# Kernel optimization log

Hardware: AMD Instinct MI355X
Metric: run time of the kernel (lower is better)

## Reference

```python
import jax, jax.numpy as jnp
import numpy as np

H, W = 256, 256
S, S_IDX, END_BIAS = 48, 3, 10
E_IDX = S - END_BIAS          # 38
N_ITER = E_IDX - (S_IDX + 1)  # 34 sequential segments after the start segment
OUT_WIN = 10                  # outlier1d window length
OUT_THRESH = 2.0


def setup_inputs() -> dict:
    key = jax.random.key(0)
    # (x, y) event coordinates in [0, W) x [0, H); t/p/b columns are unused by the module.
    events = jax.random.uniform(key, (16, 960000, 2), jnp.float32, minval=0.0, maxval=256.0)
    return {"events": events}


def _blur(a):
    """5x5 uniform (0.04) blur, SAME padding; a: [B, S, D] -> [B, S, D]."""
    k = jnp.full((1, 1, 5, 5), 0.04, jnp.float32)
    return jax.lax.conv_general_dilated(a[:, None], k, (1, 1), [(2, 2), (2, 2)])[:, 0]


def _outlier_flags(m):
    """outlier1d(m[b, si:si+10], thresh=2)[0] for si in [S_IDX+1, E_IDX). m: [B,S] -> bool [B,N_ITER]."""
    widx = (jnp.arange(N_ITER)[:, None] + S_IDX + 1) + jnp.arange(OUT_WIN)[None, :]
    w = m[:, widx]                                   # [B, N_ITER, 10]
    med = jnp.median(w, axis=-1, keepdims=True)
    diff = jnp.abs(w - med)
    mad = jnp.median(diff, axis=-1)                  # [B, N_ITER]
    return 0.6745 * diff[..., 0] / mad > OUT_THRESH


def reference(events):
    B, N, _ = events.shape
    segmentLen = N // S            # static python int
    Nu = segmentLen * S
    x = events[:, :Nu, 0].astype(jnp.int32)   # [B, Nu]
    y = events[:, :Nu, 1].astype(jnp.int32)
    chunks = jnp.repeat(jnp.arange(S), segmentLen)   # segment id per event, [Nu]
    bidx = jnp.arange(B)[:, None]

    # per-batch x-t / y-t histograms via scatter-add
    alongX = jnp.zeros((B, S, W), jnp.float32).at[bidx, chunks[None, :], x].add(1.0)
    alongY = jnp.zeros((B, S, H), jnp.float32).at[bidx, chunks[None, :], y].add(1.0)

    def proc_axis(along, D):
        flat = along.reshape(B, -1)
        cv = (flat.mean(-1) + 3.0 * jnp.std(flat, axis=-1, ddof=1))[:, None, None]
        a = _blur(jnp.clip(along, 0.0, cv))
        m = jnp.einsum('bsd,d->bs', a, jnp.arange(D, dtype=jnp.float32)) / segmentLen
        start = m[:, S_IDX:S_IDX + 1]
        aligned = jnp.round(m - start - (D // 2 - start)).astype(jnp.int32)
        return m, aligned

    meanX, alignedX = proc_axis(alongX, W)
    meanY, alignedY = proc_axis(alongY, H)
    is_out = _outlier_flags(meanX) | _outlier_flags(meanY)   # [B, N_ITER]

    def per_batch(xb, yb, aX, aY, outb):
        xs = jnp.clip(xb - aX[chunks], 0, W - 1)
        ys = jnp.clip(yb - aY[chunks], 0, H - 1)
        idx_c = (xs + W * ys).reshape(S, segmentLen)
        idx_v = (xs // 2 + (W // 2) * (ys // 2)).reshape(S, segmentLen)
        container0 = jnp.zeros(W * H, jnp.int32).at[idx_c[S_IDX]].add(1)
        ver0 = jnp.zeros((W // 2) * (H // 2), bool).at[idx_v[S_IDX]].set(True)

        def step(carry, inp):
            container, ver, stopped = carry
            ic, iv, is_o = inp
            ver_new = ver.at[iv].set(True)
            cnt = jnp.sum(ver_new).astype(jnp.float32)
            new_info = jnp.sum(jnp.logical_xor(ver_new, ver)).astype(jnp.float32)
            brk = new_info / cnt < 0.1
            do = (~stopped) & (~is_o) & (~brk)
            stopped = stopped | ((~stopped) & (~is_o) & brk)
            container = jnp.where(do, container.at[ic].add(1), container)
            ver = jnp.where(do, ver_new, ver)
            return (container, ver, stopped), None

        (container, _, _), _ = jax.lax.scan(
            step, (container0, ver0, jnp.array(False)),
            (idx_c[S_IDX + 1:E_IDX], idx_v[S_IDX + 1:E_IDX], outb))
        c = container.astype(jnp.float32)
        cv = c.mean() + 3.0 * jnp.std(c, ddof=1)
        return jnp.clip(c, 0.0, cv) / cv

    containers = jax.vmap(per_batch)(x, y, alignedX, alignedY, is_out)  # [B, W*H]
    return containers.reshape(B, 1, H, W)
```

## Files before the change

kernel.cpp:

```cpp
#include <hip/hip_runtime.h>

#define NB 16
#define NEV 960000
#define NS 48
#define SEG 20000
#define S_IDX 3
#define E_IDX 38
#define N_ITER 34
#define ND 256
#define NCH 35

__global__ __launch_bounds__(256) void hist_kernel(const float* __restrict__ events,
                                                   float* __restrict__ alongX,
                                                   float* __restrict__ alongY,
                                                   unsigned* __restrict__ compact,
                                                   unsigned* __restrict__ container,
                                                   unsigned long long* __restrict__ sums) {
    __shared__ unsigned hx[4][ND], hy[4][ND];
    int tid = threadIdx.x;
    int blk = blockIdx.x;
    int b = blk / NS, c = blk % NS;
    int wave = tid >> 6;
    #pragma unroll
    for (int j = 0; j < 4; j++) { hx[j][tid] = 0; hy[j][tid] = 0; }
    {
        uint4 z = {0u, 0u, 0u, 0u};
        for (int i = blk * 256 + tid; i < 262144; i += NB * NS * 256)
            ((uint4*)container)[i] = z;
        if (blk == 0 && tid < NB * 2) sums[tid] = 0ull;
    }
    __syncthreads();
    size_t base = (size_t)b * NEV + (size_t)c * SEG;
    const float4* ev4 = (const float4*)(events + base * 2);
    bool wr = (c >= S_IDX && c < E_IDX);
    uint2* dst = wr ? (uint2*)(compact + ((size_t)b * NCH + (c - S_IDX)) * (SEG / 2)) : nullptr;
    unsigned* HX = hx[wave];
    unsigned* HY = hy[wave];
    for (int k = tid; k < SEG / 4; k += 256) {
        float4 v0 = ev4[2 * k], v1 = ev4[2 * k + 1];
        int x0 = (int)v0.x, y0 = (int)v0.y, x1 = (int)v0.z, y1 = (int)v0.w;
        int x2 = (int)v1.x, y2 = (int)v1.y, x3 = (int)v1.z, y3 = (int)v1.w;
        x0 = x0 > 255 ? 255 : x0; y0 = y0 > 255 ? 255 : y0;
        x1 = x1 > 255 ? 255 : x1; y1 = y1 > 255 ? 255 : y1;
        x2 = x2 > 255 ? 255 : x2; y2 = y2 > 255 ? 255 : y2;
        x3 = x3 > 255 ? 255 : x3; y3 = y3 > 255 ? 255 : y3;
        atomicAdd(&HX[x0], 1u); atomicAdd(&HY[y0], 1u);
        atomicAdd(&HX[x1], 1u); atomicAdd(&HY[y1], 1u);
        atomicAdd(&HX[x2], 1u); atomicAdd(&HY[y2], 1u);
        atomicAdd(&HX[x3], 1u); atomicAdd(&HY[y3], 1u);
        if (wr) {
            uint2 p;
            p.x = (unsigned)(x0 | (y0 << 8)) | ((unsigned)(x1 | (y1 << 8)) << 16);
            p.y = (unsigned)(x2 | (y2 << 8)) | ((unsigned)(x3 | (y3 << 8)) << 16);
            dst[k] = p;
        }
    }
    __syncthreads();
    unsigned sx = hx[0][tid] + hx[1][tid] + hx[2][tid] + hx[3][tid];
    unsigned sy = hy[0][tid] + hy[1][tid] + hy[2][tid] + hy[3][tid];
    int o = (b * NS + c) * ND + tid;
    alongX[o] = (float)sx;
    alongY[o] = (float)sy;
}

__global__ __launch_bounds__(256) void stats_kernel(const float* __restrict__ alongX,
                                                    const float* __restrict__ alongY,
                                                    int* __restrict__ alignedX,
                                                    int* __restrict__ alignedY,
                                                    float* __restrict__ m_all) {
    __shared__ float sbuf[NS * ND];
    __shared__ double sredA[4], sredB[4];
    __shared__ float scv;
    int tid = threadIdx.x;
    int b = blockIdx.x >> 1, axis = blockIdx.x & 1;
    const float* along = (axis ? alongY : alongX) + (size_t)b * NS * ND;
    for (int k = 0; k < NS; k++) sbuf[k * ND + tid] = along[k * ND + tid];
    __syncthreads();
    double s = 0.0, s2 = 0.0;
    for (int k = 0; k < NS; k++) { double v = sbuf[k * ND + tid]; s += v; s2 += v * v; }
    for (int off = 32; off; off >>= 1) { s += __shfl_down(s, off); s2 += __shfl_down(s2, off); }
    if ((tid & 63) == 0) { sredA[tid >> 6] = s; sredB[tid >> 6] = s2; }
    __syncthreads();
    if (tid == 0) {
        double ts = sredA[0] + sredA[1] + sredA[2] + sredA[3];
        double ts2 = sredB[0] + sredB[1] + sredB[2] + sredB[3];
        const double N = (double)(NS * ND);
        double mean = ts / N;
        double var  = (ts2 - ts * ts / N) / (N - 1.0);
        scv = (float)(mean + 3.0 * sqrt(var));
    }
    __syncthreads();
    float cv = scv;
    int wave = tid >> 6, lane = tid & 63;
    for (int q = 0; q < 12; ++q) {
        int sI = wave * 12 + q;
        double acc = 0.0;
        #pragma unroll
        for (int k = 0; k < 4; ++k) {
            int d = lane + 64 * k;
            int lo = d - 2 < 0 ? 0 : d - 2;
            int hi = d + 2 > 255 ? 255 : d + 2;
            double Wd = 0.5 * (double)(lo + hi) * (double)(hi - lo + 1);
            double t = 0.0;
            #pragma unroll
            for (int ds = -2; ds <= 2; ++ds) {
                int ss = sI + ds;
                if (ss >= 0 && ss < NS) t += (double)fminf(sbuf[ss * ND + d], cv);
            }
            acc += t * Wd;
        }
        for (int off = 32; off; off >>= 1) acc += __shfl_down(acc, off);
        if (lane == 0) {
            float mf = (float)(acc * 0.04 / (double)SEG);
            m_all[(b * 2 + axis) * NS + sI] = mf;
            (axis ? alignedY : alignedX)[b * NS + sI] = (int)rintf(mf - 128.0f);
        }
    }
}

__global__ __launch_bounds__(256) void mask_kernel(const unsigned* __restrict__ compact,
                                                   const int* __restrict__ alignedX,
                                                   const int* __restrict__ alignedY,
                                                   unsigned* __restrict__ masks) {
    __shared__ unsigned sm[512];
    int tid = threadIdx.x, blk = blockIdx.x;
    int b = blk / NCH, ci = blk % NCH, si = S_IDX + ci;
    sm[tid] = 0; sm[tid + 256] = 0;
    __syncthreads();
    int aX = alignedX[b * NS + si], aY = alignedY[b * NS + si];
    const uint4* cp = (const uint4*)(compact + ((size_t)b * NCH + ci) * (SEG / 2));
    for (int i = tid; i < SEG / 8; i += 256) {
        uint4 w = cp[i];
        unsigned ws[4] = {w.x, w.y, w.z, w.w};
        #pragma unroll
        for (int j = 0; j < 4; j++) {
            unsigned v = ws[j];
            #pragma unroll
            for (int h = 0; h < 2; h++) {
                unsigned e = (h ? (v >> 16) : v) & 0xFFFFu;
                int xs = (int)(e & 255u) - aX; xs = xs < 0 ? 0 : (xs > 255 ? 255 : xs);
                int ys = (int)(e >> 8)   - aY; ys = ys < 0 ? 0 : (ys > 255 ? 255 : ys);
                int iv = (xs >> 1) | ((ys >> 1) << 7);
                atomicOr(&sm[iv >> 5], 1u << (iv & 31));
            }
        }
    }
    __syncthreads();
    unsigned* mo = masks + (size_t)blk * 512;
    mo[tid] = sm[tid];
    mo[tid + 256] = sm[tid + 256];
}

__device__ inline float median10(const float* v) {
    float w[10];
    #pragma unroll
    for (int i = 0; i < 10; i++) w[i] = v[i];
    #pragma unroll
    for (int i = 1; i < 10; i++) {
        float k = w[i]; int j = i - 1;
        while (j >= 0 && w[j] > k) { w[j + 1] = w[j]; j--; }
        w[j + 1] = k;
    }
    return 0.5f * (w[4] + w[5]);
}

__device__ inline bool outlier_flag(const float* w) {
    float med = median10(w);
    float d[10];
    #pragma unroll
    for (int i = 0; i < 10; i++) d[i] = fabsf(w[i] - med);
    float d0 = d[0];
    float mad = median10(d);
    return (0.6745f * d0 / mad) > 2.0f;
}

__device__ inline unsigned wave_sum_u32(unsigned v) {
    for (int off = 32; off; off >>= 1) v += __shfl_xor(v, off);
    return v;
}

__global__ __launch_bounds__(64) void decide_kernel(const unsigned* __restrict__ masks,
                                                    const float* __restrict__ m_all,
                                                    unsigned long long* __restrict__ commitmask) {
    int b = blockIdx.x, lane = threadIdx.x;
    const unsigned* mb = masks + (size_t)b * NCH * 512;
    uint4 v0 = ((const uint4*)mb)[lane * 2];
    uint4 v1 = ((const uint4*)mb)[lane * 2 + 1];
    const uint4* pp = (const uint4*)(mb + 512);
    uint4 p0 = pp[lane * 2], p1 = pp[lane * 2 + 1];
    bool f = false;
    if (lane < N_ITER) {
        const float* mx = m_all + b * 2 * NS;
        const float* my = mx + NS;
        f = outlier_flag(&mx[S_IDX + 1 + lane]) || outlier_flag(&my[S_IDX + 1 + lane]);
    }
    unsigned long long omask = __ballot(f);
    unsigned ver[8] = {v0.x, v0.y, v0.z, v0.w, v1.x, v1.y, v1.z, v1.w};
    unsigned pc = 0;
    #pragma unroll
    for (int j = 0; j < 8; j++) pc += __popc(ver[j]);
    unsigned cnt = wave_sum_u32(pc);
    unsigned long long cm = 1ull;
    for (int idx = 1; idx < NCH; ++idx) {
        uint4 c0 = p0, c1 = p1;
        if (idx + 1 < NCH) {
            const uint4* np = (const uint4*)(mb + (size_t)(idx + 1) * 512);
            p0 = np[lane * 2]; p1 = np[lane * 2 + 1];
        }
        unsigned del[8] = {c0.x, c0.y, c0.z, c0.w, c1.x, c1.y, c1.z, c1.w};
        unsigned nl = 0;
        #pragma unroll
        for (int j = 0; j < 8; j++) nl += __popc(del[j] & ~ver[j]);
        unsigned ni = wave_sum_u32(nl);
        bool is_o = (omask >> (idx - 1)) & 1;
        if (!is_o) {
            unsigned cn = cnt + ni;
            float ratio = (float)ni / (float)cn;
            if (ratio < 0.1f) break;
            cm |= 1ull << idx;
            cnt = cn;
            #pragma unroll
            for (int j = 0; j < 8; j++) ver[j] |= del[j];
        }
    }
    if (lane == 0) commitmask[b] = cm;
}

__global__ __launch_bounds__(256) void commit_kernel(const unsigned* __restrict__ compact,
                                                     const int* __restrict__ alignedX,
                                                     const int* __restrict__ alignedY,
                                                     const unsigned long long* __restrict__ commitmask,
                                                     unsigned* __restrict__ container) {
    int blk = blockIdx.x, tid = threadIdx.x;
    int b = blk / NCH, ci = blk % NCH;
    if (!((commitmask[b] >> ci) & 1ull)) return;
    int si = S_IDX + ci;
    int aX = alignedX[b * NS + si], aY = alignedY[b * NS + si];
    unsigned* cont = container + (size_t)b * 65536;
    const uint4* cp = (const uint4*)(compact + ((size_t)b * NCH + ci) * (SEG / 2));
    for (int i = tid; i < SEG / 8; i += 256) {
        uint4 w = cp[i];
        unsigned ws[4] = {w.x, w.y, w.z, w.w};
        #pragma unroll
        for (int j = 0; j < 4; j++) {
            unsigned v = ws[j];
            #pragma unroll
            for (int h = 0; h < 2; h++) {
                unsigned e = (h ? (v >> 16) : v) & 0xFFFFu;
                int xs = (int)(e & 255u) - aX; xs = xs < 0 ? 0 : (xs > 255 ? 255 : xs);
                int ys = (int)(e >> 8)   - aY; ys = ys < 0 ? 0 : (ys > 255 ? 255 : ys);
                atomicAdd(&cont[xs | (ys << 8)], 1u);
            }
        }
    }
}

__global__ __launch_bounds__(256) void cv_kernel(const unsigned* __restrict__ container,
                                                 unsigned long long* __restrict__ sums) {
    __shared__ unsigned long long sredA[4], sredB[4];
    int tid = threadIdx.x, blk = blockIdx.x;
    int b = blk >> 4, part = blk & 15;
    const uint4* c4 = (const uint4*)(container + (size_t)b * 65536) + part * 1024;
    unsigned long long s = 0, s2 = 0;
    for (int i = tid; i < 1024; i += 256) {
        uint4 v = c4[i];
        s  += (unsigned long long)v.x + v.y + v.z + v.w;
        s2 += (unsigned long long)v.x * v.x + (unsigned long long)v.y * v.y
            + (unsigned long long)v.z * v.z + (unsigned long long)v.w * v.w;
    }
    for (int off = 32; off; off >>= 1) { s += __shfl_down(s, off); s2 += __shfl_down(s2, off); }
    if ((tid & 63) == 0) { sredA[tid >> 6] = s; sredB[tid >> 6] = s2; }
    __syncthreads();
    if (tid == 0) {
        atomicAdd(&sums[b * 2],     sredA[0] + sredA[1] + sredA[2] + sredA[3]);
        atomicAdd(&sums[b * 2 + 1], sredB[0] + sredB[1] + sredB[2] + sredB[3]);
    }
}

__global__ __launch_bounds__(256) void finish_kernel(const unsigned* __restrict__ container,
                                                     const unsigned long long* __restrict__ sums,
                                                     float* __restrict__ out) {
    int g = blockIdx.x * 256 + threadIdx.x;
    int b = g >> 14;
    double ts  = (double)sums[b * 2];
    double ts2 = (double)sums[b * 2 + 1];
    double mean = ts / 65536.0;
    double var  = (ts2 - ts * ts / 65536.0) / 65535.0;
    float cv = (float)(mean + 3.0 * sqrt(var));
    uint4 v = ((const uint4*)container)[g];
    float4 o;
    o.x = fminf((float)v.x, cv) / cv;
    o.y = fminf((float)v.y, cv) / cv;
    o.z = fminf((float)v.z, cv) / cv;
    o.w = fminf((float)v.w, cv) / cv;
    ((float4*)out)[g] = o;
}

extern "C" void kernel_launch(void* const* d_in, const int* in_sizes, int n_in,
                              void* d_out, int out_size, void* d_ws, size_t ws_size,
                              hipStream_t stream) {
    const float* events = (const float*)d_in[0];
    float* out = (float*)d_out;
    char* ws = (char*)d_ws;

    float*    alongX    = (float*)(ws);
    float*    alongY    = (float*)(ws + 786432);
    unsigned* container = (unsigned*)(ws + 1572864);
    int*      alignedX  = (int*)(ws + 5767168);
    int*      alignedY  = (int*)(ws + 5770240);
    float*    m_all     = (float*)(ws + 5773312);
    unsigned long long* commitmask = (unsigned long long*)(ws + 5779456);
    unsigned long long* sums       = (unsigned long long*)(ws + 5779584);
    unsigned* compact   = (unsigned*)(ws + 6291456);
    unsigned* masks     = (unsigned*)(ws + 29360128);

    hist_kernel<<<NB * NS, 256, 0, stream>>>(events, alongX, alongY, compact, container, sums);
    stats_kernel<<<NB * 2, 256, 0, stream>>>(alongX, alongY, alignedX, alignedY, m_all);
    mask_kernel<<<NB * NCH, 256, 0, stream>>>(compact, alignedX, alignedY, masks);
    decide_kernel<<<NB, 64, 0, stream>>>(masks, m_all, commitmask);
    commit_kernel<<<NB * NCH, 256, 0, stream>>>(compact, alignedX, alignedY, commitmask, container);
    cv_kernel<<<NB * 16, 256, 0, stream>>>(container, sums);
    finish_kernel<<<1024, 256, 0, stream>>>(container, sums, out);
}
```

Baseline: 281.1 us.

## Fuse all pipeline stages into one cooperative kernel with grid syncs

Replaces the seven separate kernel launches (histogram, stats, mask, decide, commit, cv, finish) with a single cooperative kernel of 512 persistent blocks. The stages are separated by grid-wide synchronisation, and blocks loop over tiles inside each stage. The goal is to remove per-launch overhead and the gaps between dependent kernels. In exchange, it adds grid-sync cost, leaves many blocks idle during small stages such as stats and decide, and gives the histogram stage an uneven split of 768 tiles over 512 blocks. The old multi-kernel path is kept as a fallback when the occupancy check fails.

```diff
diff --git a/kernel.cpp b/kernel.cpp
--- a/kernel.cpp
+++ b/kernel.cpp
@@ -1,4 +1,7 @@
 #include <hip/hip_runtime.h>
+#include <hip/hip_cooperative_groups.h>
+
+namespace cg = cooperative_groups;
 
 #define NB 16
 #define NEV 960000
@@ -9,6 +12,294 @@
 #define N_ITER 34
 #define ND 256
 #define NCH 35
+#define GRID 512
+
+__device__ inline float median10(const float* v) {
+    float w[10];
+    #pragma unroll
+    for (int i = 0; i < 10; i++) w[i] = v[i];
+    #pragma unroll
+    for (int i = 1; i < 10; i++) {
+        float k = w[i]; int j = i - 1;
+        while (j >= 0 && w[j] > k) { w[j + 1] = w[j]; j--; }
+        w[j + 1] = k;
+    }
+    return 0.5f * (w[4] + w[5]);
+}
+
+__device__ inline bool outlier_flag(const float* w) {
+    float med = median10(w);
+    float d[10];
+    #pragma unroll
+    for (int i = 0; i < 10; i++) d[i] = fabsf(w[i] - med);
+    float d0 = d[0];
+    float mad = median10(d);
+    return (0.6745f * d0 / mad) > 2.0f;
+}
+
+__device__ inline unsigned wave_sum_u32(unsigned v) {
+    for (int off = 32; off; off >>= 1) v += __shfl_xor(v, off);
+    return v;
+}
+
+__global__ __launch_bounds__(256, 2)
+void fused_kernel(const float* __restrict__ events,
+                  float* __restrict__ alongX,
+                  float* __restrict__ alongY,
+                  unsigned* __restrict__ compact,
+                  unsigned* __restrict__ container,
+                  unsigned long long* __restrict__ sums,
+                  int* __restrict__ alignedX,
+                  int* __restrict__ alignedY,
+                  float* __restrict__ m_all,
+                  unsigned* __restrict__ masks,
+                  unsigned long long* __restrict__ commitmask,
+                  float* __restrict__ out) {
+    cg::grid_group grid = cg::this_grid();
+    __shared__ float sbuf[NS * ND];
+    __shared__ double sredA[4], sredB[4];
+    __shared__ unsigned long long credA[4], credB[4];
+    __shared__ float scv;
+    int tid = threadIdx.x, blk = blockIdx.x;
+
+    {
+        uint4 z = {0u, 0u, 0u, 0u};
+        for (int i = blk * 256 + tid; i < 262144; i += GRID * 256)
+            ((uint4*)container)[i] = z;
+        if (blk == 0 && tid < NB * 2) sums[tid] = 0ull;
+
+        unsigned (*hx)[ND] = (unsigned (*)[ND])sbuf;
+        unsigned (*hy)[ND] = (unsigned (*)[ND])(sbuf + 1024);
+        int wave = tid >> 6;
+        for (int tile = blk; tile < NB * NS; tile += GRID) {
+            __syncthreads();
+            #pragma unroll
+            for (int j = 0; j < 4; j++) { hx[j][tid] = 0; hy[j][tid] = 0; }
+            __syncthreads();
+            int b = tile / NS, c = tile % NS;
+            size_t base = (size_t)b * NEV + (size_t)c * SEG;
+            const float4* ev4 = (const float4*)(events + base * 2);
+            bool wr = (c >= S_IDX && c < E_IDX);
+            uint2* dst = wr ? (uint2*)(compact + ((size_t)b * NCH + (c - S_IDX)) * (SEG / 2)) : nullptr;
+            unsigned* HX = hx[wave];
+            unsigned* HY = hy[wave];
+            for (int k = tid; k < SEG / 4; k += 256) {
+                float4 v0 = ev4[2 * k], v1 = ev4[2 * k + 1];
+                int x0 = (int)v0.x, y0 = (int)v0.y, x1 = (int)v0.z, y1 = (int)v0.w;
+                int x2 = (int)v1.x, y2 = (int)v1.y, x3 = (int)v1.z, y3 = (int)v1.w;
+                x0 = x0 > 255 ? 255 : x0; y0 = y0 > 255 ? 255 : y0;
+                x1 = x1 > 255 ? 255 : x1; y1 = y1 > 255 ? 255 : y1;
+                x2 = x2 > 255 ? 255 : x2; y2 = y2 > 255 ? 255 : y2;
+                x3 = x3 > 255 ? 255 : x3; y3 = y3 > 255 ? 255 : y3;
+                atomicAdd(&HX[x0], 1u); atomicAdd(&HY[y0], 1u);
+                atomicAdd(&HX[x1], 1u); atomicAdd(&HY[y1], 1u);
+                atomicAdd(&HX[x2], 1u); atomicAdd(&HY[y2], 1u);
+                atomicAdd(&HX[x3], 1u); atomicAdd(&HY[y3], 1u);
+                if (wr) {
+                    uint2 p;
+                    p.x = (unsigned)(x0 | (y0 << 8)) | ((unsigned)(x1 | (y1 << 8)) << 16);
+                    p.y = (unsigned)(x2 | (y2 << 8)) | ((unsigned)(x3 | (y3 << 8)) << 16);
+                    dst[k] = p;
+                }
+            }
+            __syncthreads();
+            unsigned sx = hx[0][tid] + hx[1][tid] + hx[2][tid] + hx[3][tid];
+            unsigned sy = hy[0][tid] + hy[1][tid] + hy[2][tid] + hy[3][tid];
+            int o = tile * ND + tid;
+            alongX[o] = (float)sx;
+            alongY[o] = (float)sy;
+        }
+    }
+    grid.sync();
+
+    if (blk < NB * 2) {
+        int b = blk >> 1, axis = blk & 1;
+        const float* along = (axis ? alongY : alongX) + (size_t)b * NS * ND;
+        for (int k = 0; k < NS; k++) sbuf[k * ND + tid] = along[k * ND + tid];
+        __syncthreads();
+        double s = 0.0, s2 = 0.0;
+        for (int k = 0; k < NS; k++) { double v = sbuf[k * ND + tid]; s += v; s2 += v * v; }
+        for (int off = 32; off; off >>= 1) { s += __shfl_down(s, off); s2 += __shfl_down(s2, off); }
+        if ((tid & 63) == 0) { sredA[tid >> 6] = s; sredB[tid >> 6] = s2; }
+        __syncthreads();
+        if (tid == 0) {
+            double ts = sredA[0] + sredA[1] + sredA[2] + sredA[3];
+            double ts2 = sredB[0] + sredB[1] + sredB[2] + sredB[3];
+            const double N = (double)(NS * ND);
+            double mean = ts / N;
+            double var  = (ts2 - ts * ts / N) / (N - 1.0);
+            scv = (float)(mean + 3.0 * sqrt(var));
+        }
+        __syncthreads();
+        float cv = scv;
+        int wave = tid >> 6, lane = tid & 63;
+        for (int q = 0; q < 12; ++q) {
+            int sI = wave * 12 + q;
+            double acc = 0.0;
+            #pragma unroll
+            for (int k = 0; k < 4; ++k) {
+                int d = lane + 64 * k;
+                int lo = d - 2 < 0 ? 0 : d - 2;
+                int hi = d + 2 > 255 ? 255 : d + 2;
+                double Wd = 0.5 * (double)(lo + hi) * (double)(hi - lo + 1);
+                double t = 0.0;
+                #pragma unroll
+                for (int ds = -2; ds <= 2; ++ds) {
+                    int ss = sI + ds;
+                    if (ss >= 0 && ss < NS) t += (double)fminf(sbuf[ss * ND + d], cv);
+                }
+                acc += t * Wd;
+            }
+            for (int off = 32; off; off >>= 1) acc += __shfl_down(acc, off);
+            if (lane == 0) {
+                float mf = (float)(acc * 0.04 / (double)SEG);
+                m_all[(b * 2 + axis) * NS + sI] = mf;
+                (axis ? alignedY : alignedX)[b * NS + sI] = (int)rintf(mf - 128.0f);
+            }
+        }
+    }
+    grid.sync();
+
+    {
+        unsigned* sm = (unsigned*)sbuf;
+        for (int tile = blk; tile < NB * NCH; tile += GRID) {
+            __syncthreads();
+            sm[tid] = 0; sm[tid + 256] = 0;
+            __syncthreads();
+            int b = tile / NCH, ci = tile % NCH, si = S_IDX + ci;
+            int aX = alignedX[b * NS + si], aY = alignedY[b * NS + si];
+            const uint4* cp = (const uint4*)(compact + ((size_t)b * NCH + ci) * (SEG / 2));
+            for (int i = tid; i < SEG / 8; i += 256) {
+                uint4 w = cp[i];
+                unsigned wsv[4] = {w.x, w.y, w.z, w.w};
+                #pragma unroll
+                for (int j = 0; j < 4; j++) {
+                    unsigned v = wsv[j];
+                    #pragma unroll
+                    for (int h = 0; h < 2; h++) {
+                        unsigned e = (h ? (v >> 16) : v) & 0xFFFFu;
+                        int xs = (int)(e & 255u) - aX; xs = xs < 0 ? 0 : (xs > 255 ? 255 : xs);
+                        int ys = (int)(e >> 8)   - aY; ys = ys < 0 ? 0 : (ys > 255 ? 255 : ys);
+                        int iv = (xs >> 1) | ((ys >> 1) << 7);
+                        atomicOr(&sm[iv >> 5], 1u << (iv & 31));
+                    }
+                }
+            }
+            __syncthreads();
+            unsigned* mo = masks + (size_t)tile * 512;
+            mo[tid] = sm[tid];
+            mo[tid + 256] = sm[tid + 256];
+        }
+    }
+    grid.sync();
+
+    if (blk < NB && tid < 64) {
+        int b = blk, lane = tid;
+        const unsigned* mb = masks + (size_t)b * NCH * 512;
+        uint4 v0 = ((const uint4*)mb)[lane * 2];
+        uint4 v1 = ((const uint4*)mb)[lane * 2 + 1];
+        const uint4* pp = (const uint4*)(mb + 512);
+        uint4 p0 = pp[lane * 2], p1 = pp[lane * 2 + 1];
+        bool f = false;
+        if (lane < N_ITER) {
+            const float* mx = m_all + b * 2 * NS;
+            const float* my = mx + NS;
+            f = outlier_flag(&mx[S_IDX + 1 + lane]) || outlier_flag(&my[S_IDX + 1 + lane]);
+        }
+        unsigned long long omask = __ballot(f);
+        unsigned ver[8] = {v0.x, v0.y, v0.z, v0.w, v1.x, v1.y, v1.z, v1.w};
+        unsigned pc = 0;
+        #pragma unroll
+        for (int j = 0; j < 8; j++) pc += __popc(ver[j]);
+        unsigned cnt = wave_sum_u32(pc);
+        unsigned long long cm = 1ull;
+        for (int idx = 1; idx < NCH; ++idx) {
+            uint4 c0 = p0, c1 = p1;
+            if (idx + 1 < NCH) {
+                const uint4* np = (const uint4*)(mb + (size_t)(idx + 1) * 512);
+                p0 = np[lane * 2]; p1 = np[lane * 2 + 1];
+            }
+            unsigned del[8] = {c0.x, c0.y, c0.z, c0.w, c1.x, c1.y, c1.z, c1.w};
+            unsigned nl = 0;
+            #pragma unroll
+            for (int j = 0; j < 8; j++) nl += __popc(del[j] & ~ver[j]);
+            unsigned ni = wave_sum_u32(nl);
+            bool is_o = (omask >> (idx - 1)) & 1;
+            if (!is_o) {
+                unsigned cn = cnt + ni;
+                float ratio = (float)ni / (float)cn;
+                if (ratio < 0.1f) break;
+                cm |= 1ull << idx;
+                cnt = cn;
+                #pragma unroll
+                for (int j = 0; j < 8; j++) ver[j] |= del[j];
+            }
+        }
+        if (lane == 0) commitmask[b] = cm;
+    }
+    grid.sync();
+
+    for (int tile = blk; tile < NB * NCH; tile += GRID) {
+        int b = tile / NCH, ci = tile % NCH;
+        if (!((commitmask[b] >> ci) & 1ull)) continue;
+        int si = S_IDX + ci;
+        int aX = alignedX[b * NS + si], aY = alignedY[b * NS + si];
+        unsigned* cont = container + (size_t)b * 65536;
+        const uint4* cp = (const uint4*)(compact + ((size_t)b * NCH + ci) * (SEG / 2));
+        for (int i = tid; i < SEG / 8; i += 256) {
+            uint4 w = cp[i];
+            unsigned wsv[4] = {w.x, w.y, w.z, w.w};
+            #pragma unroll
+            for (int j = 0; j < 4; j++) {
+                unsigned v = wsv[j];
+                #pragma unroll
+                for (int h = 0; h < 2; h++) {
+                    unsigned e = (h ? (v >> 16) : v) & 0xFFFFu;
+                    int xs = (int)(e & 255u) - aX; xs = xs < 0 ? 0 : (xs > 255 ? 255 : xs);
+                    int ys = (int)(e >> 8)   - aY; ys = ys < 0 ? 0 : (ys > 255 ? 255 : ys);
+                    atomicAdd(&cont[xs | (ys << 8)], 1u);
+                }
+            }
+        }
+    }
+    grid.sync();
+
+    if (blk < NB * 16) {
+        int b = blk >> 4, part = blk & 15;
+        const uint4* c4 = (const uint4*)(container + (size_t)b * 65536) + part * 1024;
+        unsigned long long s = 0, s2 = 0;
+        for (int i = tid; i < 1024; i += 256) {
+            uint4 v = c4[i];
+            s  += (unsigned long long)v.x + v.y + v.z + v.w;
+            s2 += (unsigned long long)v.x * v.x + (unsigned long long)v.y * v.y
+                + (unsigned long long)v.z * v.z + (unsigned long long)v.w * v.w;
+        }
+        for (int off = 32; off; off >>= 1) { s += __shfl_down(s, off); s2 += __shfl_down(s2, off); }
+        if ((tid & 63) == 0) { credA[tid >> 6] = s; credB[tid >> 6] = s2; }
+        __syncthreads();
+        if (tid == 0) {
+            atomicAdd(&sums[b * 2],     credA[0] + credA[1] + credA[2] + credA[3]);
+            atomicAdd(&sums[b * 2 + 1], credB[0] + credB[1] + credB[2] + credB[3]);
+        }
+    }
+    grid.sync();
+
+    for (int g = blk * 256 + tid; g < 262144; g += GRID * 256) {
+        int b = g >> 14;
+        double ts  = (double)sums[b * 2];
+        double ts2 = (double)sums[b * 2 + 1];
+        double mean = ts / 65536.0;
+        double var  = (ts2 - ts * ts / 65536.0) / 65535.0;
+        float cv = (float)(mean + 3.0 * sqrt(var));
+        uint4 v = ((const uint4*)container)[g];
+        float4 o;
+        o.x = fminf((float)v.x, cv) / cv;
+        o.y = fminf((float)v.y, cv) / cv;
+        o.z = fminf((float)v.z, cv) / cv;
+        o.w = fminf((float)v.w, cv) / cv;
+        ((float4*)out)[g] = o;
+    }
+}
 
 __global__ __launch_bounds__(256) void hist_kernel(const float* __restrict__ events,
                                                    float* __restrict__ alongX,
@@ -131,10 +422,10 @@
     const uint4* cp = (const uint4*)(compact + ((size_t)b * NCH + ci) * (SEG / 2));
     for (int i = tid; i < SEG / 8; i += 256) {
         uint4 w = cp[i];
-        unsigned ws[4] = {w.x, w.y, w.z, w.w};
+        unsigned wsv[4] = {w.x, w.y, w.z, w.w};
         #pragma unroll
         for (int j = 0; j < 4; j++) {
-            unsigned v = ws[j];
+            unsigned v = wsv[j];
             #pragma unroll
             for (int h = 0; h < 2; h++) {
                 unsigned e = (h ? (v >> 16) : v) & 0xFFFFu;
@@ -149,34 +440,6 @@
     unsigned* mo = masks + (size_t)blk * 512;
     mo[tid] = sm[tid];
     mo[tid + 256] = sm[tid + 256];
-}
-
-__device__ inline float median10(const float* v) {
-    float w[10];
-    #pragma unroll
-    for (int i = 0; i < 10; i++) w[i] = v[i];
-    #pragma unroll
-    for (int i = 1; i < 10; i++) {
-        float k = w[i]; int j = i - 1;
-        while (j >= 0 && w[j] > k) { w[j + 1] = w[j]; j--; }
-        w[j + 1] = k;
-    }
-    return 0.5f * (w[4] + w[5]);
-}
-
-__device__ inline bool outlier_flag(const float* w) {
-    float med = median10(w);
-    float d[10];
-    #pragma unroll
-    for (int i = 0; i < 10; i++) d[i] = fabsf(w[i] - med);
-    float d0 = d[0];
-    float mad = median10(d);
-    return (0.6745f * d0 / mad) > 2.0f;
-}
-
-__device__ inline unsigned wave_sum_u32(unsigned v) {
-    for (int off = 32; off; off >>= 1) v += __shfl_xor(v, off);
-    return v;
 }
 
 __global__ __launch_bounds__(64) void decide_kernel(const unsigned* __restrict__ masks,
@@ -240,10 +503,10 @@
     const uint4* cp = (const uint4*)(compact + ((size_t)b * NCH + ci) * (SEG / 2));
     for (int i = tid; i < SEG / 8; i += 256) {
         uint4 w = cp[i];
-        unsigned ws[4] = {w.x, w.y, w.z, w.w};
+        unsigned wsv[4] = {w.x, w.y, w.z, w.w};
         #pragma unroll
         for (int j = 0; j < 4; j++) {
-            unsigned v = ws[j];
+            unsigned v = wsv[j];
             #pragma unroll
             for (int h = 0; h < 2; h++) {
                 unsigned e = (h ? (v >> 16) : v) & 0xFFFFu;
@@ -314,11 +577,24 @@
     unsigned* compact   = (unsigned*)(ws + 6291456);
     unsigned* masks     = (unsigned*)(ws + 29360128);
 
-    hist_kernel<<<NB * NS, 256, 0, stream>>>(events, alongX, alongY, compact, container, sums);
-    stats_kernel<<<NB * 2, 256, 0, stream>>>(alongX, alongY, alignedX, alignedY, m_all);
-    mask_kernel<<<NB * NCH, 256, 0, stream>>>(compact, alignedX, alignedY, masks);
-    decide_kernel<<<NB, 64, 0, stream>>>(masks, m_all, commitmask);
-    commit_kernel<<<NB * NCH, 256, 0, stream>>>(compact, alignedX, alignedY, commitmask, container);
-    cv_kernel<<<NB * 16, 256, 0, stream>>>(container, sums);
-    finish_kernel<<<1024, 256, 0, stream>>>(container, sums, out);
-}
+    int maxBlocksPerCU = 0;
+    hipError_t occ_err = hipOccupancyMaxActiveBlocksPerMultiprocessor(
+        &maxBlocksPerCU, (const void*)fused_kernel, 256, 0);
+    bool coop_ok = (occ_err == hipSuccess) && (maxBlocksPerCU * 256 >= GRID);
+
+    if (coop_ok) {
+        void* args[] = {(void*)&events, (void*)&alongX, (void*)&alongY, (void*)&compact,
+                        (void*)&container, (void*)&sums, (void*)&alignedX, (void*)&alignedY,
+                        (void*)&m_all, (void*)&masks, (void*)&commitmask, (void*)&out};
+        hipLaunchCooperativeKernel((const void*)fused_kernel, dim3(GRID), dim3(256),
+                                   args, 0, stream);
+    } else {
+        hist_kernel<<<NB * NS, 256, 0, stream>>>(events, alongX, alongY, compact, container, sums);
+        stats_kernel<<<NB * 2, 256, 0, stream>>>(alongX, alongY, alignedX, alignedY, m_all);
+        mask_kernel<<<NB * NCH, 256, 0, stream>>>(compact, alignedX, alignedY, masks);
+        decide_kernel<<<NB, 64, 0, stream>>>(masks, m_all, commitmask);
+        commit_kernel<<<NB * NCH, 256, 0, stream>>>(compact, alignedX, alignedY, commitmask, container);
+        cv_kernel<<<NB * 16, 256, 0, stream>>>(container, sums);
+        finish_kernel<<<1024, 256, 0, stream>>>(container, sums, out);
+    }
+}
```

New measurement: 587.3 us. 2.09x slower.

## Split stats, mask and commit kernels across more blocks; fuse sum-of-squares into histogram

Applied to the files above, without the earlier changes.

The histogram kernel now processes 8 events per thread, writes 16-byte packed compact records, zeroes the mask buffer, and atomically accumulates per-batch sum of squares. The stats kernel uses those sums, with the total count fixed at 960000, so it no longer does its own pass. Its blur-and-mean work is split into four row groups per batch and axis, which raises the block count from 32 to 128. The mask and commit kernels are split into 2 and 4 sub-blocks per segment, which adds global atomicOr merges into the masks in exchange for more parallelism on a GPU that was underfilled.

```diff
diff --git a/kernel.cpp b/kernel.cpp
--- a/kernel.cpp
+++ b/kernel.cpp
@@ -15,43 +15,61 @@
                                                    float* __restrict__ alongY,
                                                    unsigned* __restrict__ compact,
                                                    unsigned* __restrict__ container,
-                                                   unsigned long long* __restrict__ sums) {
+                                                   unsigned* __restrict__ masks,
+                                                   unsigned long long* __restrict__ sums,
+                                                   unsigned long long* __restrict__ cvsums) {
     __shared__ unsigned hx[4][ND], hy[4][ND];
+    __shared__ unsigned long long qredX[4], qredY[4];
     int tid = threadIdx.x;
     int blk = blockIdx.x;
     int b = blk / NS, c = blk % NS;
-    int wave = tid >> 6;
+    int wave = tid >> 6, lane = tid & 63;
     #pragma unroll
     for (int j = 0; j < 4; j++) { hx[j][tid] = 0; hy[j][tid] = 0; }
     {
         uint4 z = {0u, 0u, 0u, 0u};
         for (int i = blk * 256 + tid; i < 262144; i += NB * NS * 256)
             ((uint4*)container)[i] = z;
+        for (int i = blk * 256 + tid; i < 71680; i += NB * NS * 256)
+            ((uint4*)masks)[i] = z;
         if (blk == 0 && tid < NB * 2) sums[tid] = 0ull;
+        if (blk == 1 && tid < NB * 2) cvsums[tid] = 0ull;
     }
     __syncthreads();
     size_t base = (size_t)b * NEV + (size_t)c * SEG;
     const float4* ev4 = (const float4*)(events + base * 2);
     bool wr = (c >= S_IDX && c < E_IDX);
-    uint2* dst = wr ? (uint2*)(compact + ((size_t)b * NCH + (c - S_IDX)) * (SEG / 2)) : nullptr;
+    uint4* dst = wr ? (uint4*)(compact + ((size_t)b * NCH + (c - S_IDX)) * (SEG / 2)) : nullptr;
     unsigned* HX = hx[wave];
     unsigned* HY = hy[wave];
-    for (int k = tid; k < SEG / 4; k += 256) {
-        float4 v0 = ev4[2 * k], v1 = ev4[2 * k + 1];
+    for (int k = tid; k < SEG / 8; k += 256) {
+        float4 v0 = ev4[4 * k], v1 = ev4[4 * k + 1], v2 = ev4[4 * k + 2], v3 = ev4[4 * k + 3];
         int x0 = (int)v0.x, y0 = (int)v0.y, x1 = (int)v0.z, y1 = (int)v0.w;
         int x2 = (int)v1.x, y2 = (int)v1.y, x3 = (int)v1.z, y3 = (int)v1.w;
+        int x4 = (int)v2.x, y4 = (int)v2.y, x5 = (int)v2.z, y5 = (int)v2.w;
+        int x6 = (int)v3.x, y6 = (int)v3.y, x7 = (int)v3.z, y7 = (int)v3.w;
         x0 = x0 > 255 ? 255 : x0; y0 = y0 > 255 ? 255 : y0;
         x1 = x1 > 255 ? 255 : x1; y1 = y1 > 255 ? 255 : y1;
         x2 = x2 > 255 ? 255 : x2; y2 = y2 > 255 ? 255 : y2;
         x3 = x3 > 255 ? 255 : x3; y3 = y3 > 255 ? 255 : y3;
+        x4 = x4 > 255 ? 255 : x4; y4 = y4 > 255 ? 255 : y4;
+        x5 = x5 > 255 ? 255 : x5; y5 = y5 > 255 ? 255 : y5;
+        x6 = x6 > 255 ? 255 : x6; y6 = y6 > 255 ? 255 : y6;
+        x7 = x7 > 255 ? 255 : x7; y7 = y7 > 255 ? 255 : y7;
         atomicAdd(&HX[x0], 1u); atomicAdd(&HY[y0], 1u);
         atomicAdd(&HX[x1], 1u); atomicAdd(&HY[y1], 1u);
         atomicAdd(&HX[x2], 1u); atomicAdd(&HY[y2], 1u);
         atomicAdd(&HX[x3], 1u); atomicAdd(&HY[y3], 1u);
+        atomicAdd(&HX[x4], 1u); atomicAdd(&HY[y4], 1u);
+        atomicAdd(&HX[x5], 1u); atomicAdd(&HY[y5], 1u);
+        atomicAdd(&HX[x6], 1u); atomicAdd(&HY[y6], 1u);
+        atomicAdd(&HX[x7], 1u); atomicAdd(&HY[y7], 1u);
         if (wr) {
-            uint2 p;
+            uint4 p;
             p.x = (unsigned)(x0 | (y0 << 8)) | ((unsigned)(x1 | (y1 << 8)) << 16);
             p.y = (unsigned)(x2 | (y2 << 8)) | ((unsigned)(x3 | (y3 << 8)) << 16);
+            p.z = (unsigned)(x4 | (y4 << 8)) | ((unsigned)(x5 | (y5 << 8)) << 16);
+            p.w = (unsigned)(x6 | (y6 << 8)) | ((unsigned)(x7 | (y7 << 8)) << 16);
             dst[k] = p;
         }
     }
@@ -61,39 +79,43 @@
     int o = (b * NS + c) * ND + tid;
     alongX[o] = (float)sx;
     alongY[o] = (float)sy;
+    unsigned long long qx = (unsigned long long)sx * sx;
+    unsigned long long qy = (unsigned long long)sy * sy;
+    for (int off = 32; off; off >>= 1) { qx += __shfl_down(qx, off); qy += __shfl_down(qy, off); }
+    if (lane == 0) { qredX[wave] = qx; qredY[wave] = qy; }
+    __syncthreads();
+    if (tid == 0) {
+        atomicAdd(&cvsums[b * 2],     qredX[0] + qredX[1] + qredX[2] + qredX[3]);
+        atomicAdd(&cvsums[b * 2 + 1], qredY[0] + qredY[1] + qredY[2] + qredY[3]);
+    }
 }
 
 __global__ __launch_bounds__(256) void stats_kernel(const float* __restrict__ alongX,
                                                     const float* __restrict__ alongY,
+                                                    const unsigned long long* __restrict__ cvsums,
                                                     int* __restrict__ alignedX,
                                                     int* __restrict__ alignedY,
                                                     float* __restrict__ m_all) {
-    __shared__ float sbuf[NS * ND];
-    __shared__ double sredA[4], sredB[4];
-    __shared__ float scv;
+    __shared__ float sbuf[16 * ND];
     int tid = threadIdx.x;
-    int b = blockIdx.x >> 1, axis = blockIdx.x & 1;
+    int blk = blockIdx.x;
+    int g = blk & 3, axis = (blk >> 2) & 1, b = blk >> 3;
     const float* along = (axis ? alongY : alongX) + (size_t)b * NS * ND;
-    for (int k = 0; k < NS; k++) sbuf[k * ND + tid] = along[k * ND + tid];
-    __syncthreads();
-    double s = 0.0, s2 = 0.0;
-    for (int k = 0; k < NS; k++) { double v = sbuf[k * ND + tid]; s += v; s2 += v * v; }
-    for (int off = 32; off; off >>= 1) { s += __shfl_down(s, off); s2 += __shfl_down(s2, off); }
-    if ((tid & 63) == 0) { sredA[tid >> 6] = s; sredB[tid >> 6] = s2; }
-    __syncthreads();
-    if (tid == 0) {
-        double ts = sredA[0] + sredA[1] + sredA[2] + sredA[3];
-        double ts2 = sredB[0] + sredB[1] + sredB[2] + sredB[3];
-        const double N = (double)(NS * ND);
-        double mean = ts / N;
-        double var  = (ts2 - ts * ts / N) / (N - 1.0);
-        scv = (float)(mean + 3.0 * sqrt(var));
-    }
-    __syncthreads();
-    float cv = scv;
+    int rbase = g * 12 - 2;
+    for (int j = 0; j < 16; j++) {
+        int r = rbase + j;
+        if (r >= 0 && r < NS) sbuf[j * ND + tid] = along[r * ND + tid];
+    }
+    double ts  = 960000.0;
+    double ts2 = (double)cvsums[b * 2 + axis];
+    const double N = (double)(NS * ND);
+    double mean = ts / N;
+    double var  = (ts2 - ts * ts / N) / (N - 1.0);
+    float cv = (float)(mean + 3.0 * sqrt(var));
+    __syncthreads();
     int wave = tid >> 6, lane = tid & 63;
-    for (int q = 0; q < 12; ++q) {
-        int sI = wave * 12 + q;
+    for (int q = 0; q < 3; ++q) {
+        int sI = g * 12 + wave * 3 + q;
         double acc = 0.0;
         #pragma unroll
         for (int k = 0; k < 4; ++k) {
@@ -105,7 +127,7 @@
             #pragma unroll
             for (int ds = -2; ds <= 2; ++ds) {
                 int ss = sI + ds;
-                if (ss >= 0 && ss < NS) t += (double)fminf(sbuf[ss * ND + d], cv);
+                if (ss >= 0 && ss < NS) t += (double)fminf(sbuf[(ss - rbase) * ND + d], cv);
             }
             acc += t * Wd;
         }
@@ -124,17 +146,19 @@
                                                    unsigned* __restrict__ masks) {
     __shared__ unsigned sm[512];
     int tid = threadIdx.x, blk = blockIdx.x;
-    int b = blk / NCH, ci = blk % NCH, si = S_IDX + ci;
+    int hi = blk & 1;
+    int tile = blk >> 1;
+    int b = tile / NCH, ci = tile % NCH, si = S_IDX + ci;
     sm[tid] = 0; sm[tid + 256] = 0;
     __syncthreads();
     int aX = alignedX[b * NS + si], aY = alignedY[b * NS + si];
     const uint4* cp = (const uint4*)(compact + ((size_t)b * NCH + ci) * (SEG / 2));
-    for (int i = tid; i < SEG / 8; i += 256) {
+    for (int i = hi * 1250 + tid; i < (hi + 1) * 1250; i += 256) {
         uint4 w = cp[i];
-        unsigned ws[4] = {w.x, w.y, w.z, w.w};
+        unsigned wsv[4] = {w.x, w.y, w.z, w.w};
         #pragma unroll
         for (int j = 0; j < 4; j++) {
-            unsigned v = ws[j];
+            unsigned v = wsv[j];
             #pragma unroll
             for (int h = 0; h < 2; h++) {
                 unsigned e = (h ? (v >> 16) : v) & 0xFFFFu;
@@ -146,9 +170,10 @@
         }
     }
     __syncthreads();
-    unsigned* mo = masks + (size_t)blk * 512;
-    mo[tid] = sm[tid];
-    mo[tid + 256] = sm[tid + 256];
+    unsigned* mo = masks + (size_t)tile * 512;
+    unsigned v0 = sm[tid], v1 = sm[tid + 256];
+    if (v0) atomicOr(&mo[tid], v0);
+    if (v1) atomicOr(&mo[tid + 256], v1);
 }
 
 __device__ inline float median10(const float* v) {
@@ -232,18 +257,20 @@
                                                      const unsigned long long* __restrict__ commitmask,
                                                      unsigned* __restrict__ container) {
     int blk = blockIdx.x, tid = threadIdx.x;
-    int b = blk / NCH, ci = blk % NCH;
+    int qi = blk & 3;
+    int tile = blk >> 2;
+    int b = tile / NCH, ci = tile % NCH;
     if (!((commitmask[b] >> ci) & 1ull)) return;
     int si = S_IDX + ci;
     int aX = alignedX[b * NS + si], aY = alignedY[b * NS + si];
     unsigned* cont = container + (size_t)b * 65536;
     const uint4* cp = (const uint4*)(compact + ((size_t)b * NCH + ci) * (SEG / 2));
-    for (int i = tid; i < SEG / 8; i += 256) {
+    for (int i = qi * 625 + tid; i < (qi + 1) * 625; i += 256) {
         uint4 w = cp[i];
-        unsigned ws[4] = {w.x, w.y, w.z, w.w};
+        unsigned wsv[4] = {w.x, w.y, w.z, w.w};
         #pragma unroll
         for (int j = 0; j < 4; j++) {
-            unsigned v = ws[j];
+            unsigned v = wsv[j];
             #pragma unroll
             for (int h = 0; h < 2; h++) {
                 unsigned e = (h ? (v >> 16) : v) & 0xFFFFu;
@@ -311,14 +338,18 @@
     float*    m_all     = (float*)(ws + 5773312);
     unsigned long long* commitmask = (unsigned long long*)(ws + 5779456);
     unsigned long long* sums       = (unsigned long long*)(ws + 5779584);
+    unsigned long long* cvsums     = (unsigned long long*)(ws + 5779840);
     unsigned* compact   = (unsigned*)(ws + 6291456);
     unsigned* masks     = (unsigned*)(ws + 29360128);
 
-    hist_kernel<<<NB * NS, 256, 0, stream>>>(events, alongX, alongY, compact, container, sums);
-    stats_kernel<<<NB * 2, 256, 0, stream>>>(alongX, alongY, alignedX, alignedY, m_all);
-    mask_kernel<<<NB * NCH, 256, 0, stream>>>(compact, alignedX, alignedY, masks);
+    hist_kernel<<<NB * NS, 256, 0, stream>>>(events, alongX, alongY, compact,
+                                             container, masks, sums, cvsums);
+    stats_kernel<<<NB * 2 * 4, 256, 0, stream>>>(alongX, alongY, cvsums,
+                                                 alignedX, alignedY, m_all);
+    mask_kernel<<<NB * NCH * 2, 256, 0, stream>>>(compact, alignedX, alignedY, masks);
     decide_kernel<<<NB, 64, 0, stream>>>(masks, m_all, commitmask);
-    commit_kernel<<<NB * NCH, 256, 0, stream>>>(compact, alignedX, alignedY, commitmask, container);
+    commit_kernel<<<NB * NCH * 4, 256, 0, stream>>>(compact, alignedX, alignedY,
+                                                    commitmask, container);
     cv_kernel<<<NB * 16, 256, 0, stream>>>(container, sums);
     finish_kernel<<<1024, 256, 0, stream>>>(container, sums, out);
 }
```

Result: faster. 269.6 us (-4.1%).
